# Kernel optimization log

Hardware: AMD Instinct MI355X
Metric: run time of the kernel (lower is better)

## Reference

```python
import jax, jax.numpy as jnp
import numpy as np

NEG_SLOPE = 0.2

def setup_inputs() -> dict:
    key = jax.random.key(0)
    ks = jax.random.split(key, 6)
    N, C, H, E_DIM, E = 50000, 128, 64, 16, 800000
    x = jax.random.normal(ks[0], (N, C), dtype=jnp.float32)
    edge_index = jax.random.randint(ks[1], (2, E), 0, N, dtype=jnp.int64)
    edge_attr = jax.random.normal(ks[2], (E, E_DIM), dtype=jnp.float32)
    fc_w = jax.random.normal(ks[3], (H, C), dtype=jnp.float32) * (1.0 / np.sqrt(C))
    fc_b = jnp.zeros((H,), dtype=jnp.float32)
    att_w = jax.random.normal(ks[4], (H, 2 * H + E_DIM), dtype=jnp.float32) * (1.0 / np.sqrt(2 * H + E_DIM))
    att_b = jnp.zeros((H,), dtype=jnp.float32)
    return {"x": x, "edge_index": edge_index, "edge_attr": edge_attr,
            "fc_w": fc_w, "fc_b": fc_b, "att_w": att_w, "att_b": att_b}

def reference(x, edge_index, edge_attr, fc_w, fc_b, att_w, att_b):
    # Node projection: h = fc(x), [N, H]
    h = x @ fc_w.T + fc_b
    src = edge_index[0]  # i (destination of aggregation)
    dst = edge_index[1]  # j (neighbor whose features are aggregated)
    h_i = h[src]                      # [E, H]
    h_j = h[dst]                      # [E, H]
    feat = jnp.concatenate([h_i, h_j, edge_attr], axis=-1)  # [E, 2H+edge_dim]
    alpha = jax.nn.leaky_relu(feat @ att_w.T + att_b, negative_slope=NEG_SLOPE)  # [E, H]
    # dropout is identity in eval mode (training=False)
    msg = h_j * alpha                 # [E, H]
    out = jax.ops.segment_sum(msg, src, num_segments=h.shape[0])  # scatter-add into out[i]
    return out
```

## Files before the change

kernel.cpp:

```cpp
#include <hip/hip_runtime.h>


__device__ __forceinline__ unsigned bf16r(float f) {
    unsigned u = __float_as_uint(f);
    return (u + 0x7fffu + ((u >> 16) & 1u)) >> 16;
}
__device__ __forceinline__ float bf_lo(unsigned p) { return __uint_as_float(p << 16); }
__device__ __forceinline__ float bf_hi(unsigned p) { return __uint_as_float(p & 0xffff0000u); }

__global__ __launch_bounds__(256) void node_kernel(
    const float* __restrict__ x,
    const float* __restrict__ fc_w, const float* __restrict__ fc_b,
    const float* __restrict__ att_w, const float* __restrict__ att_b,
    float* __restrict__ ai_out, unsigned* __restrict__ hj_out, int N)
{
    __shared__ __align__(16) float4 wF[64 * 32];
    __shared__ __align__(16) float4 wI[64 * 16];
    __shared__ __align__(16) float4 wJ[64 * 16];
    __shared__ __align__(16) float xs[4][128];
    __shared__ __align__(16) float hs[4][64];

    const int t = threadIdx.x;
    for (int idx = t; idx < 64 * 32; idx += 256) {
        int l = idx >> 5, c = idx & 31;
        wF[l * 32 + (c ^ (l & 31))] =
            *reinterpret_cast<const float4*>(fc_w + l * 128 + c * 4);
    }
    for (int idx = t; idx < 64 * 16; idx += 256) {
        int l = idx >> 4, c = idx & 15;
        wI[l * 16 + (c ^ (l & 15))] =
            *reinterpret_cast<const float4*>(att_w + l * 144 + c * 4);
        wJ[l * 16 + (c ^ (l & 15))] =
            *reinterpret_cast<const float4*>(att_w + l * 144 + 64 + c * 4);
    }
    __syncthreads();

    const int w = t >> 6, l = t & 63;
    const float bF = fc_b[l];
    const float bA = att_b[l];
    const int waveId = blockIdx.x * 4 + w;
    const int nWaves = gridDim.x * 4;

    for (int n = waveId; n < N; n += nWaves) {
        float2 xv = reinterpret_cast<const float2*>(x)[(size_t)n * 64 + l];
        xs[w][2 * l] = xv.x;
        xs[w][2 * l + 1] = xv.y;
        float acc = bF;
        #pragma unroll
        for (int c = 0; c < 32; ++c) {
            float4 wv = wF[l * 32 + (c ^ (l & 31))];
            float4 xc = *reinterpret_cast<const float4*>(&xs[w][c * 4]);
            acc = fmaf(wv.x, xc.x, acc);
            acc = fmaf(wv.y, xc.y, acc);
            acc = fmaf(wv.z, xc.z, acc);
            acc = fmaf(wv.w, xc.w, acc);
        }
        hs[w][l] = acc;
        float a2 = bA, a3 = 0.f;
        #pragma unroll
        for (int c = 0; c < 16; ++c) {
            float4 hvv = *reinterpret_cast<const float4*>(&hs[w][c * 4]);
            float4 wi = wI[l * 16 + (c ^ (l & 15))];
            float4 wj = wJ[l * 16 + (c ^ (l & 15))];
            a2 = fmaf(wi.x, hvv.x, a2); a2 = fmaf(wi.y, hvv.y, a2);
            a2 = fmaf(wi.z, hvv.z, a2); a2 = fmaf(wi.w, hvv.w, a2);
            a3 = fmaf(wj.x, hvv.x, a3); a3 = fmaf(wj.y, hvv.y, a3);
            a3 = fmaf(wj.z, hvv.z, a3); a3 = fmaf(wj.w, hvv.w, a3);
        }
        ai_out[(size_t)n * 64 + l] = a2;
        hj_out[(size_t)n * 64 + l] = (bf16r(a3) << 16) | bf16r(acc);
    }
}

__global__ __launch_bounds__(256) void hist_kernel(
    const int* __restrict__ ei, int* __restrict__ count, int E)
{
    int i = blockIdx.x * 256 + threadIdx.x;
    int stride = gridDim.x * 256;
    for (; i < E; i += stride) atomicAdd(&count[ei[i]], 1);
}

__global__ __launch_bounds__(1024) void scan_kernel(
    const int* __restrict__ count, int* __restrict__ start, int N)
{
    __shared__ int wsums[16];
    const int t = threadIdx.x, lane = t & 63, w = t >> 6;
    int carry = 0;
    for (int base = 0; base < N; base += 1024) {
        int i = base + t;
        int c = (i < N) ? count[i] : 0;
        int v = c;
        #pragma unroll
        for (int off = 1; off < 64; off <<= 1) {
            int u = __shfl_up(v, off);
            if (lane >= off) v += u;
        }
        if (lane == 63) wsums[w] = v;
        __syncthreads();
        int wbase = 0, total = 0;
        #pragma unroll
        for (int q = 0; q < 16; ++q) {
            int s = wsums[q];
            if (q < w) wbase += s;
            total += s;
        }
        if (i < N) start[i] = carry + wbase + v - c;
        carry += total;
        __syncthreads();
    }
}

__global__ __launch_bounds__(256) void scatter_kernel(
    const int* __restrict__ ei, int* __restrict__ start,
    int* __restrict__ sd, uint4* __restrict__ eaS,
    const float4* __restrict__ ea4, int E)
{
    int i = blockIdx.x * 256 + threadIdx.x;
    int stride = gridDim.x * 256;
    for (; i < E; i += stride) {
        int s = ei[i];
        int pos = atomicAdd(&start[s], 1);
        sd[pos] = ei[E + i];
        float4 r0 = ea4[(size_t)i * 4 + 0], r1 = ea4[(size_t)i * 4 + 1];
        float4 r2 = ea4[(size_t)i * 4 + 2], r3 = ea4[(size_t)i * 4 + 3];
        uint4 q0 = make_uint4((bf16r(r0.y) << 16) | bf16r(r0.x),
                              (bf16r(r0.w) << 16) | bf16r(r0.z),
                              (bf16r(r1.y) << 16) | bf16r(r1.x),
                              (bf16r(r1.w) << 16) | bf16r(r1.z));
        uint4 q1 = make_uint4((bf16r(r2.y) << 16) | bf16r(r2.x),
                              (bf16r(r2.w) << 16) | bf16r(r2.z),
                              (bf16r(r3.y) << 16) | bf16r(r3.x),
                              (bf16r(r3.w) << 16) | bf16r(r3.z));
        eaS[(size_t)pos * 2 + 0] = q0;
        eaS[(size_t)pos * 2 + 1] = q1;
    }
}

__global__ __launch_bounds__(256) void csr_edge_kernel(
    const int* __restrict__ sd, const uint2* __restrict__ eaS2,
    const int* __restrict__ endp, const int* __restrict__ count,
    const float* __restrict__ ai, const unsigned* __restrict__ hj,
    const float* __restrict__ att_w, float* __restrict__ out, int N)
{
    __shared__ uint2 eas[4][256];
    __shared__ float weS[64][17];

    const int t = threadIdx.x, w = t >> 6, l = t & 63;
    for (int idx = t; idx < 1024; idx += 256)
        weS[idx >> 4][idx & 15] = att_w[(idx >> 4) * 144 + 128 + (idx & 15)];
    __syncthreads();

    const int n = blockIdx.x * 4 + w;
    if (n >= N) return;

    float we[16];
    #pragma unroll
    for (int k = 0; k < 16; ++k) we[k] = weS[l][k];

    const int deg = count[n];
    const int base = endp[n] - deg;
    const float aiv = ai[(size_t)n * 64 + l];
    float acc = 0.f;

#define EDGE_BODY(KK, UU)                                                      \
    {                                                                          \
        float pre = aiv + bf_hi(UU);                                           \
        _Pragma("unroll") for (int r = 0; r < 4; ++r) {                        \
            uint2 q = eas[w][(KK) * 4 + r];                                    \
            pre = fmaf(we[r * 4 + 0], bf_lo(q.x), pre);                        \
            pre = fmaf(we[r * 4 + 1], bf_hi(q.x), pre);                        \
            pre = fmaf(we[r * 4 + 2], bf_lo(q.y), pre);                        \
            pre = fmaf(we[r * 4 + 3], bf_hi(q.y), pre);                        \
        }                                                                      \
        float alpha = pre > 0.f ? pre : 0.2f * pre;                            \
        acc = fmaf(bf_lo(UU), alpha, acc);                                     \
    }

    int done = 0;
    while (done < deg) {
        const int rem = min(64, deg - done);
        int v = 0;
        if (l < rem) v = sd[base + done + l];
        for (int f = l; f < rem * 4; f += 64)
            eas[w][f] = eaS2[(size_t)(base + done) * 4 + f];
        int k = 0;
        for (; k + 8 <= rem; k += 8) {
            int d[8]; unsigned u[8];
            #pragma unroll
            for (int j = 0; j < 8; ++j) {
                d[j] = __shfl(v, k + j);
                u[j] = hj[(size_t)d[j] * 64 + l];
            }
            #pragma unroll
            for (int j = 0; j < 8; ++j) EDGE_BODY(k + j, u[j]);
        }
        for (; k < rem; ++k) {
            int dd = __shfl(v, k);
            unsigned uu = hj[(size_t)dd * 64 + l];
            EDGE_BODY(k, uu);
        }
        done += rem;
    }
#undef EDGE_BODY
    out[(size_t)n * 64 + l] = acc;
}

extern "C" void kernel_launch(void* const* d_in, const int* in_sizes, int n_in,
                              void* d_out, int out_size, void* d_ws, size_t ws_size,
                              hipStream_t stream) {
    const float* x     = (const float*)d_in[0];
    const int*   ei    = (const int*)d_in[1];
    const float* ea    = (const float*)d_in[2];
    const float* fc_w  = (const float*)d_in[3];
    const float* fc_b  = (const float*)d_in[4];
    const float* att_w = (const float*)d_in[5];
    const float* att_b = (const float*)d_in[6];
    float* out = (float*)d_out;

    const int N = in_sizes[0] / 128;
    const int E = in_sizes[2] / 16;

    char* p = (char*)d_ws;
    auto align256 = [](size_t v) { return (v + 255) & ~(size_t)255; };
    float*    ai    = (float*)p;        p += align256((size_t)N * 64 * 4);
    unsigned* hj    = (unsigned*)p;     p += align256((size_t)N * 64 * 4);
    int*      count = (int*)p;          p += align256((size_t)N * 4);
    int*      startp= (int*)p;          p += align256((size_t)N * 4);
    int*      sd    = (int*)p;          p += align256((size_t)E * 4);
    uint4*    eaS   = (uint4*)p;

    hipMemsetAsync(count, 0, (size_t)N * sizeof(int), stream);

    node_kernel<<<512, 256, 0, stream>>>(x, fc_w, fc_b, att_w, att_b, ai, hj, N);
    hist_kernel<<<1024, 256, 0, stream>>>(ei, count, E);
    scan_kernel<<<1, 1024, 0, stream>>>(count, startp, N);
    scatter_kernel<<<1024, 256, 0, stream>>>(ei, startp, sd, eaS,
                                             (const float4*)ea, E);
    csr_edge_kernel<<<(N + 3) / 4, 256, 0, stream>>>(
        sd, (const uint2*)eaS, startp, count, ai, hj, att_w, out, N);
}
```

Before: 264.2 us.

## Parallelize prefix scan across blocks and split edge-attr reorder into gather pass

After: 253.6 us. -4.0%, faster.

```diff
diff --git a/kernel.cpp b/kernel.cpp
--- a/kernel.cpp
+++ b/kernel.cpp
@@ -80,64 +80,105 @@
     for (; i < E; i += stride) atomicAdd(&count[ei[i]], 1);
 }
 
-__global__ __launch_bounds__(1024) void scan_kernel(
-    const int* __restrict__ count, int* __restrict__ start, int N)
-{
-    __shared__ int wsums[16];
-    const int t = threadIdx.x, lane = t & 63, w = t >> 6;
-    int carry = 0;
-    for (int base = 0; base < N; base += 1024) {
-        int i = base + t;
-        int c = (i < N) ? count[i] : 0;
-        int v = c;
-        #pragma unroll
-        for (int off = 1; off < 64; off <<= 1) {
-            int u = __shfl_up(v, off);
-            if (lane >= off) v += u;
-        }
-        if (lane == 63) wsums[w] = v;
-        __syncthreads();
-        int wbase = 0, total = 0;
-        #pragma unroll
-        for (int q = 0; q < 16; ++q) {
-            int s = wsums[q];
-            if (q < w) wbase += s;
-            total += s;
-        }
-        if (i < N) start[i] = carry + wbase + v - c;
-        carry += total;
-        __syncthreads();
+__global__ __launch_bounds__(256) void scan1_kernel(
+    const int* __restrict__ count, int* __restrict__ start,
+    int* __restrict__ bsum, int N)
+{
+    __shared__ int wsum[4];
+    const int t = threadIdx.x, blk = blockIdx.x;
+    const int idx0 = blk * 1024 + t * 4;
+    int c0 = 0, c1 = 0, c2 = 0, c3 = 0;
+    if (idx0 + 3 < N) {
+        int4 c = *reinterpret_cast<const int4*>(count + idx0);
+        c0 = c.x; c1 = c.y; c2 = c.z; c3 = c.w;
+    } else {
+        if (idx0 + 0 < N) c0 = count[idx0 + 0];
+        if (idx0 + 1 < N) c1 = count[idx0 + 1];
+        if (idx0 + 2 < N) c2 = count[idx0 + 2];
+    }
+    const int s = c0 + c1 + c2 + c3;
+    const int lane = t & 63, w = t >> 6;
+    int v = s;
+    #pragma unroll
+    for (int off = 1; off < 64; off <<= 1) {
+        int u = __shfl_up(v, off);
+        if (lane >= off) v += u;
+    }
+    if (lane == 63) wsum[w] = v;
+    __syncthreads();
+    int base = 0;
+    if (w > 0) base += wsum[0];
+    if (w > 1) base += wsum[1];
+    if (w > 2) base += wsum[2];
+    const int excl = base + v - s;
+    if (idx0 + 0 < N) start[idx0 + 0] = excl;
+    if (idx0 + 1 < N) start[idx0 + 1] = excl + c0;
+    if (idx0 + 2 < N) start[idx0 + 2] = excl + c0 + c1;
+    if (idx0 + 3 < N) start[idx0 + 3] = excl + c0 + c1 + c2;
+    if (t == 255) bsum[blk] = base + v;
+}
+
+__global__ void scan2_kernel(int* __restrict__ bsum, int nb)
+{
+    const int l = threadIdx.x;
+    int v = (l < nb) ? bsum[l] : 0;
+    int inc = v;
+    #pragma unroll
+    for (int off = 1; off < 64; off <<= 1) {
+        int u = __shfl_up(inc, off);
+        if (l >= off) inc += u;
+    }
+    if (l < nb) bsum[l] = inc - v;
+}
+
+__global__ __launch_bounds__(256) void scan3_kernel(
+    int* __restrict__ start, const int* __restrict__ bsum, int N)
+{
+    const int blk = blockIdx.x;
+    const int add = bsum[blk];
+    #pragma unroll
+    for (int q = 0; q < 4; ++q) {
+        int i = blk * 1024 + q * 256 + threadIdx.x;
+        if (i < N) start[i] += add;
     }
 }
 
 __global__ __launch_bounds__(256) void scatter_kernel(
     const int* __restrict__ ei, int* __restrict__ start,
-    int* __restrict__ sd, uint4* __restrict__ eaS,
-    const float4* __restrict__ ea4, int E)
+    int2* __restrict__ sd, int E)
 {
     int i = blockIdx.x * 256 + threadIdx.x;
     int stride = gridDim.x * 256;
     for (; i < E; i += stride) {
         int s = ei[i];
         int pos = atomicAdd(&start[s], 1);
-        sd[pos] = ei[E + i];
-        float4 r0 = ea4[(size_t)i * 4 + 0], r1 = ea4[(size_t)i * 4 + 1];
-        float4 r2 = ea4[(size_t)i * 4 + 2], r3 = ea4[(size_t)i * 4 + 3];
-        uint4 q0 = make_uint4((bf16r(r0.y) << 16) | bf16r(r0.x),
-                              (bf16r(r0.w) << 16) | bf16r(r0.z),
-                              (bf16r(r1.y) << 16) | bf16r(r1.x),
-                              (bf16r(r1.w) << 16) | bf16r(r1.z));
-        uint4 q1 = make_uint4((bf16r(r2.y) << 16) | bf16r(r2.x),
-                              (bf16r(r2.w) << 16) | bf16r(r2.z),
-                              (bf16r(r3.y) << 16) | bf16r(r3.x),
-                              (bf16r(r3.w) << 16) | bf16r(r3.z));
-        eaS[(size_t)pos * 2 + 0] = q0;
-        eaS[(size_t)pos * 2 + 1] = q1;
-    }
+        sd[pos] = make_int2(ei[E + i], i);
+    }
+}
+
+__global__ __launch_bounds__(256) void reorder_kernel(
+    const int2* __restrict__ sd, const float4* __restrict__ ea4,
+    uint4* __restrict__ eaS, int E)
+{
+    int j = blockIdx.x * 256 + threadIdx.x;
+    if (j >= E) return;
+    int eid = sd[j].y;
+    float4 r0 = ea4[(size_t)eid * 4 + 0], r1 = ea4[(size_t)eid * 4 + 1];
+    float4 r2 = ea4[(size_t)eid * 4 + 2], r3 = ea4[(size_t)eid * 4 + 3];
+    uint4 q0 = make_uint4((bf16r(r0.y) << 16) | bf16r(r0.x),
+                          (bf16r(r0.w) << 16) | bf16r(r0.z),
+                          (bf16r(r1.y) << 16) | bf16r(r1.x),
+                          (bf16r(r1.w) << 16) | bf16r(r1.z));
+    uint4 q1 = make_uint4((bf16r(r2.y) << 16) | bf16r(r2.x),
+                          (bf16r(r2.w) << 16) | bf16r(r2.z),
+                          (bf16r(r3.y) << 16) | bf16r(r3.x),
+                          (bf16r(r3.w) << 16) | bf16r(r3.z));
+    eaS[(size_t)j * 2 + 0] = q0;
+    eaS[(size_t)j * 2 + 1] = q1;
 }
 
 __global__ __launch_bounds__(256) void csr_edge_kernel(
-    const int* __restrict__ sd, const uint2* __restrict__ eaS2,
+    const int2* __restrict__ sd, const uint2* __restrict__ eaS2,
     const int* __restrict__ endp, const int* __restrict__ count,
     const float* __restrict__ ai, const unsigned* __restrict__ hj,
     const float* __restrict__ att_w, float* __restrict__ out, int N)
@@ -180,7 +221,7 @@
     while (done < deg) {
         const int rem = min(64, deg - done);
         int v = 0;
-        if (l < rem) v = sd[base + done + l];
+        if (l < rem) v = sd[base + done + l].x;
         for (int f = l; f < rem * 4; f += 64)
             eas[w][f] = eaS2[(size_t)(base + done) * 4 + f];
         int k = 0;
@@ -226,16 +267,23 @@
     unsigned* hj    = (unsigned*)p;     p += align256((size_t)N * 64 * 4);
     int*      count = (int*)p;          p += align256((size_t)N * 4);
     int*      startp= (int*)p;          p += align256((size_t)N * 4);
-    int*      sd    = (int*)p;          p += align256((size_t)E * 4);
+    int*      bsum  = (int*)p;          p += align256(64 * 4);
+    int2*     sd    = (int2*)p;         p += align256((size_t)E * 8);
     uint4*    eaS   = (uint4*)p;
 
     hipMemsetAsync(count, 0, (size_t)N * sizeof(int), stream);
 
     node_kernel<<<512, 256, 0, stream>>>(x, fc_w, fc_b, att_w, att_b, ai, hj, N);
     hist_kernel<<<1024, 256, 0, stream>>>(ei, count, E);
-    scan_kernel<<<1, 1024, 0, stream>>>(count, startp, N);
-    scatter_kernel<<<1024, 256, 0, stream>>>(ei, startp, sd, eaS,
-                                             (const float4*)ea, E);
+
+    const int nb1 = (N + 1023) / 1024;
+    scan1_kernel<<<nb1, 256, 0, stream>>>(count, startp, bsum, N);
+    scan2_kernel<<<1, 64, 0, stream>>>(bsum, nb1);
+    scan3_kernel<<<nb1, 256, 0, stream>>>(startp, bsum, N);
+
+    scatter_kernel<<<1024, 256, 0, stream>>>(ei, startp, sd, E);
+    reorder_kernel<<<(E + 255) / 256, 256, 0, stream>>>(sd, (const float4*)ea, eaS, E);
+
     csr_edge_kernel<<<(N + 3) / 4, 256, 0, stream>>>(
         sd, (const uint2*)eaS, startp, count, ai, hj, att_w, out, N);
 }
```
